# Optimization experiments

Measured on AMD Instinct MI355X. Metric: run time of the kernel, lower is better.

The kernel has to match this reference:

```python
import jax, jax.numpy as jnp
import numpy as np

B, S, D, H = 4, 2048, 1024, 16
HS = D // H  # head size = 64


def setup_inputs() -> dict:
    key = jax.random.key(0)
    k1, k2, k3 = jax.random.split(key, 3)
    return {
        "input_data": jax.random.normal(k1, (B, S, D), dtype=jnp.float32),
        "w_qkv": jax.random.normal(k2, (D, 3 * D), dtype=jnp.float32) * (1.0 / np.sqrt(D)),
        "b_qkv": jnp.zeros((3 * D,), dtype=jnp.float32),
        "w_proj": jax.random.normal(k3, (D, D), dtype=jnp.float32) * (1.0 / np.sqrt(D)),
        "b_proj": jnp.zeros((D,), dtype=jnp.float32),
    }


def reference(input_data, w_qkv, b_qkv, w_proj, b_proj):
    b, s, d = input_data.shape
    qkv = input_data @ w_qkv + b_qkv  # [b, s, 3d]
    q, k, v = jnp.split(qkv, 3, axis=-1)
    # [b, h, s, hs]
    q = q.reshape(b, s, H, HS).transpose(0, 2, 1, 3)
    k = k.reshape(b, s, H, HS).transpose(0, 2, 1, 3)
    v = v.reshape(b, s, H, HS).transpose(0, 2, 1, 3)
    # NB: original module scales by 1/sqrt(num_heads), not 1/sqrt(head_size)
    scores = jnp.einsum('bhqd,bhkd->bhqk', q, k) / jnp.sqrt(jnp.float32(H))
    causal = jnp.tril(jnp.ones((s, s), dtype=bool))
    scores = jnp.where(causal[None, None], scores, -jnp.inf)
    weights = jax.nn.softmax(scores, axis=-1)  # dropout p=0.0 -> identity
    out = jnp.einsum('bhqk,bhkd->bhqd', weights, v)
    out = out.transpose(0, 2, 1, 3).reshape(b, s, d)
    return out @ w_proj + b_proj
```

## Files before the change

### kernel.cpp

```cpp
#include <hip/hip_runtime.h>


typedef unsigned short u16;
typedef short bf16x8 __attribute__((ext_vector_type(8)));
typedef unsigned short u16x8 __attribute__((ext_vector_type(8)));
typedef float f32x4 __attribute__((ext_vector_type(4)));
typedef float f32x16 __attribute__((ext_vector_type(16)));

#define S_LEN 2048
#define DMODEL 1024
#define NHEAD 16
#define MROWS 8192

#define SCALE_LOG2E 0.36067376022224085f
#define DEFER_THR 8.0f

__device__ __forceinline__ u16 f2bf(float f) {
  union { float f; unsigned u; } c; c.f = f;
  unsigned u = c.u;
  u += 0x7fffu + ((u >> 16) & 1u);
  return (u16)(u >> 16);
}

__device__ __forceinline__ float exp2_fast(float x) {
  float r; asm("v_exp_f32 %0, %1" : "=v"(r) : "v"(x)); return r;
}

__device__ __forceinline__ unsigned cvtpk_bf16(float a, float b) {
  unsigned r;
  asm("v_cvt_pk_bf16_f32 %0, %1, %2" : "=v"(r) : "v"(a), "v"(b));
  return r;
}

__device__ __forceinline__ void plswap(unsigned& a, unsigned& b) {
  asm("v_permlane32_swap_b32 %0, %1" : "+v"(a), "+v"(b));
}

__device__ __forceinline__ f32x4 mfma16(bf16x8 a, bf16x8 b, f32x4 c) {
  return __builtin_amdgcn_mfma_f32_16x16x32_bf16(a, b, c, 0, 0, 0);
}

__device__ __forceinline__ f32x16 mfma32(bf16x8 a, bf16x8 b, f32x16 c) {
  return __builtin_amdgcn_mfma_f32_32x32x16_bf16(a, b, c, 0, 0, 0);
}

__device__ __forceinline__ void gload_lds16(const void* g, void* l) {
  __builtin_amdgcn_global_load_lds((__attribute__((address_space(1))) void*)g,
                                   (__attribute__((address_space(3))) void*)l,
                                   16, 0, 0);
}

__global__ void k_f32_to_bf16(const float* __restrict__ in, u16* __restrict__ out, int n) {
  int i = (blockIdx.x * 256 + threadIdx.x) * 4;
  if (i < n) {
    float4 v = *reinterpret_cast<const float4*>(in + i);
    ushort4 o;
    o.x = f2bf(v.x); o.y = f2bf(v.y); o.z = f2bf(v.z); o.w = f2bf(v.w);
    *reinterpret_cast<ushort4*>(out + i) = o;
  }
}

__global__ void k_transpose_to_bf16(const float* __restrict__ in, u16* __restrict__ out,
                                    int K, int N) {
  __shared__ float t[32][33];
  int n0 = blockIdx.x * 32, k0 = blockIdx.y * 32;
  int tx = threadIdx.x & 31, ty = threadIdx.x >> 5;
#pragma unroll
  for (int i = 0; i < 32; i += 8)
    t[ty + i][tx] = in[(size_t)(k0 + ty + i) * N + n0 + tx];
  __syncthreads();
#pragma unroll
  for (int i = 0; i < 32; i += 8)
    out[(size_t)(n0 + ty + i) * K + k0 + tx] = f2bf(t[tx][ty + i]);
}

template <int MODE>
__global__ __launch_bounds__(256) void k_gemm_bt(const u16* __restrict__ A,
                                                 const u16* __restrict__ Bt,
                                                 const float* __restrict__ bias,
                                                 u16* __restrict__ outb,
                                                 float* __restrict__ outf,
                                                 u16* __restrict__ vtout,
                                                 int N, int K) {
  __shared__ u16 As[128 * 64];
  __shared__ u16 Bs[128 * 64];
  const int tid = threadIdx.x;
  const int lane = tid & 63, wave = tid >> 6;
  const int wm = wave >> 1, wn = wave & 1;
  const int lr = lane & 15, lk = lane >> 4;
  const int m0 = blockIdx.x * 128, n0 = blockIdx.y * 128;

  f32x4 zero4 = {0.f, 0.f, 0.f, 0.f};
  f32x4 acc[4][4];
#pragma unroll
  for (int m = 0; m < 4; ++m)
#pragma unroll
    for (int n = 0; n < 4; ++n) acc[m][n] = zero4;

  const int nkt = K >> 6;
  for (int kt = 0; kt < nkt; ++kt) {
    const u16* Ag = A + (size_t)m0 * K + kt * 64;
    const u16* Bg = Bt + (size_t)n0 * K + kt * 64;
#pragma unroll
    for (int j = 0; j < 4; ++j) {
      int chunk = j * 4 + wave;
      int row = chunk * 8 + (lane >> 3);
      int cole = (lane & 7) * 8;
      gload_lds16(Ag + (size_t)row * K + cole, &As[chunk * 512]);
      gload_lds16(Bg + (size_t)row * K + cole, &Bs[chunk * 512]);
    }
    __syncthreads();
#pragma unroll
    for (int ks = 0; ks < 2; ++ks) {
      bf16x8 af[4], bfr[4];
#pragma unroll
      for (int m = 0; m < 4; ++m)
        af[m] = *reinterpret_cast<const bf16x8*>(&As[(wm * 64 + m * 16 + lr) * 64 + ks * 32 + lk * 8]);
#pragma unroll
      for (int n = 0; n < 4; ++n)
        bfr[n] = *reinterpret_cast<const bf16x8*>(&Bs[(wn * 64 + n * 16 + lr) * 64 + ks * 32 + lk * 8]);
#pragma unroll
      for (int m = 0; m < 4; ++m)
#pragma unroll
        for (int n = 0; n < 4; ++n) acc[m][n] = mfma16(af[m], bfr[n], acc[m][n]);
    }
    __syncthreads();
  }

#pragma unroll
  for (int n = 0; n < 4; ++n) {
    int col = n0 + wn * 64 + n * 16 + lr;
    float bv = bias[col];
#pragma unroll
    for (int m = 0; m < 4; ++m) {
      int rowb = m0 + wm * 64 + m * 16 + lk * 4;
      if (MODE == 1) {
#pragma unroll
        for (int r = 0; r < 4; ++r)
          outf[(size_t)(rowb + r) * N + col] = acc[m][n][r] + bv;
      } else {
        if (col < 2048) {
#pragma unroll
          for (int r = 0; r < 4; ++r)
            outb[(size_t)(rowb + r) * 2048 + col] = f2bf(acc[m][n][r] + bv);
        } else {
          int hh = (col >> 6) & 15, dd = col & 63;
          int bb = rowb >> 11, ss = rowb & 2047;
          ushort4 o;
          o.x = f2bf(acc[m][n][0] + bv);
          o.y = f2bf(acc[m][n][1] + bv);
          o.z = f2bf(acc[m][n][2] + bv);
          o.w = f2bf(acc[m][n][3] + bv);
          *reinterpret_cast<ushort4*>(
              vtout + ((size_t)(bb * 16 + hh) * 64 + dd) * 2048 + ss) = o;
        }
      }
    }
  }
}

__global__ __launch_bounds__(256, 2) void k_attn5(const u16* __restrict__ qk,
                                                  const u16* __restrict__ vt,
                                                  u16* __restrict__ ao) {
  __shared__ u16 Ks[2][4096];
  __shared__ u16 Vs[2][4096];

  const int tid = threadIdx.x;
  const int lane = tid & 63, wave = tid >> 6;
  const int l31 = lane & 31, hi = lane >> 5;
  const int gid = blockIdx.x;
  const int bh = gid & 63;
  const int tq = gid >> 6;
  const int qb = (tq < 4) ? tq : 11 - tq;
  const int b = bh >> 4, h = bh & 15;

  const int qlo0 = qb * 128 + wave * 32;
  const int qhi0 = 1920 - qb * 128 + wave * 32;
  const int ktd_lo = qlo0 >> 6;
  const int ktd_hi = qhi0 >> 6;
  const int KTMAX = 31 - 2 * qb;
  const int qrel0 = qlo0 + l31 - ktd_lo * 64;
  const int qrel1 = qhi0 + l31 - ktd_hi * 64;

  bf16x8 qf[2][4];
  {
    const u16* q0p = qk + ((size_t)b * S_LEN + qlo0 + l31) * 2048 + h * 64 + hi * 8;
    const u16* q1p = qk + ((size_t)b * S_LEN + qhi0 + l31) * 2048 + h * 64 + hi * 8;
#pragma unroll
    for (int ks = 0; ks < 4; ++ks) {
      qf[0][ks] = *reinterpret_cast<const bf16x8*>(q0p + ks * 16);
      qf[1][ks] = *reinterpret_cast<const bf16x8*>(q1p + ks * 16);
    }
  }

  const int swzcol = 16 * ((lane & 7) ^ (lane >> 3));
  const char* kg = (const char*)qk + ((size_t)b * S_LEN) * 4096 + 2048 + h * 128 +
                   (size_t)(lane >> 3) * 4096 + swzcol;
  const char* vg = (const char*)vt + ((size_t)bh * 64 + (lane >> 3)) * 4096 + swzcol;

#define STAGE(BUF, KT)                                                              \
  {                                                                                 \
    const char* kg_ = kg + (size_t)(KT) * 64 * 4096;                                \
    const char* vg_ = vg + (size_t)(KT) * 128;                                      \
    gload_lds16(kg_ + (size_t)(wave * 8) * 4096, &Ks[BUF][wave * 512]);             \
    gload_lds16(kg_ + (size_t)((wave + 4) * 8) * 4096, &Ks[BUF][(wave + 4) * 512]); \
    gload_lds16(vg_ + (size_t)(wave * 8) * 4096, &Vs[BUF][wave * 512]);             \
    gload_lds16(vg_ + (size_t)((wave + 4) * 8) * 4096, &Vs[BUF][(wave + 4) * 512]); \
  }

  f32x16 oT[2][2];
#pragma unroll
  for (int m = 0; m < 2; ++m)
#pragma unroll
    for (int kb = 0; kb < 2; ++kb)
#pragma unroll
      for (int g = 0; g < 16; ++g) oT[m][kb][g] = 0.f;
  float m_i[2] = {-INFINITY, -INFINITY};
  float l_i[2] = {0.f, 0.f};

  const int rsw = (l31 & 7) << 4;

#define SM32(SC, M, MASKED, QREL, FR)                                           \
  {                                                                             \
    float s_[2][16];                                                            \
    float mx_ = -INFINITY;                                                      \
    _Pragma("unroll") for (int kb = 0; kb < 2; ++kb)                            \
      _Pragma("unroll") for (int g = 0; g < 16; ++g) {                          \
        float v_ = SC[kb][g] * SCALE_LOG2E;                                     \
        if (MASKED) {                                                           \
          int key_ = kb * 32 + (g & 3) + ((g >> 2) << 3) + hi * 4;              \
          if (key_ > (QREL)) v_ = -INFINITY;                                    \
        }                                                                       \
        s_[kb][g] = v_;                                                         \
        mx_ = fmaxf(mx_, v_);                                                   \
      }                                                                         \
    mx_ = fmaxf(mx_, __shfl_xor(mx_, 32, 64));                                  \
    if (__any(mx_ > m_i[M] + DEFER_THR)) {                                      \
      float mn_ = fmaxf(m_i[M], mx_);                                           \
      float c_ = exp2_fast(m_i[M] - mn_);                                       \
      m_i[M] = mn_;                                                             \
      l_i[M] *= c_;                                                             \
      _Pragma("unroll") for (int kb = 0; kb < 2; ++kb)                          \
        _Pragma("unroll") for (int g = 0; g < 16; ++g) oT[M][kb][g] *= c_;      \
    }                                                                           \
    float rs_ = 0.f;                                                            \
    unsigned pk_[8][2];                                                         \
    _Pragma("unroll") for (int kb = 0; kb < 2; ++kb)                            \
      _Pragma("unroll") for (int s = 0; s < 4; ++s) {                           \
        float p0_ = exp2_fast(s_[kb][s * 4 + 0] - m_i[M]);                      \
        float p1_ = exp2_fast(s_[kb][s * 4 + 1] - m_i[M]);                      \
        float p2_ = exp2_fast(s_[kb][s * 4 + 2] - m_i[M]);                      \
        float p3_ = exp2_fast(s_[kb][s * 4 + 3] - m_i[M]);                      \
        rs_ += (p0_ + p1_) + (p2_ + p3_);                                       \
        pk_[kb * 4 + s][0] = cvtpk_bf16(p0_, p1_);                              \
        pk_[kb * 4 + s][1] = cvtpk_bf16(p2_, p3_);                              \
      }                                                                         \
    rs_ += __shfl_xor(rs_, 32, 64);                                             \
    l_i[M] += rs_;                                                              \
    _Pragma("unroll") for (int t = 0; t < 4; ++t) {                             \
      unsigned a0_ = pk_[2 * t][0], b0_ = pk_[2 * t + 1][0];                    \
      unsigned a1_ = pk_[2 * t][1], b1_ = pk_[2 * t + 1][1];                    \
      plswap(a0_, b0_);                                                         \
      plswap(a1_, b1_);                                                         \
      FR[t][0] = a0_; FR[t][1] = a1_; FR[t][2] = b0_; FR[t][3] = b1_;           \
    }                                                                           \
  }

  STAGE(0, 0);
  __syncthreads();
  int buf = 0;

  for (int kt = 0; kt <= KTMAX; ++kt) {
    if (kt < KTMAX) STAGE(buf ^ 1, kt + 1);

    const char* Kb = (const char*)&Ks[buf][0];
    const char* Vb = (const char*)&Vs[buf][0];
    const bool lo_act = (kt <= ktd_lo);
    const bool hi_act = (kt <= ktd_hi);
    const bool mask0 = (kt == ktd_lo), mask1 = (kt == ktd_hi);

    bf16x8 kf[2][4];
#pragma unroll
    for (int kb = 0; kb < 2; ++kb)
#pragma unroll
      for (int ks = 0; ks < 4; ++ks)
        kf[kb][ks] = *reinterpret_cast<const bf16x8*>(
            Kb + (kb * 32 + l31) * 128 + ((ks * 32 + hi * 16) ^ rsw));

    f32x16 sc0[2], sc1[2];
#pragma unroll
    for (int kb = 0; kb < 2; ++kb) {
      if (hi_act) {
        sc1[kb] = mfma32(kf[kb][0], qf[1][0], f32x16{});
#pragma unroll
        for (int ks = 1; ks < 4; ++ks) sc1[kb] = mfma32(kf[kb][ks], qf[1][ks], sc1[kb]);
      }
      if (lo_act) {
        sc0[kb] = mfma32(kf[kb][0], qf[0][0], f32x16{});
#pragma unroll
        for (int ks = 1; ks < 4; ++ks) sc0[kb] = mfma32(kf[kb][ks], qf[0][ks], sc0[kb]);
      }
    }

    bf16x8 vf[2][4];
#pragma unroll
    for (int kbd = 0; kbd < 2; ++kbd)
#pragma unroll
      for (int t = 0; t < 4; ++t)
        vf[kbd][t] = *reinterpret_cast<const bf16x8*>(
            Vb + (kbd * 32 + l31) * 128 + ((t * 32 + hi * 16) ^ rsw));

    if (lo_act) {
      unsigned fr0[4][4];
      SM32(sc0, 0, mask0, qrel0, fr0);
#pragma unroll
      for (int t = 0; t < 4; ++t) {
        bf16x8 pb = *reinterpret_cast<const bf16x8*>(&fr0[t][0]);
        oT[0][0] = mfma32(vf[0][t], pb, oT[0][0]);
        oT[0][1] = mfma32(vf[1][t], pb, oT[0][1]);
      }
    }
    if (hi_act) {
      unsigned fr1[4][4];
      SM32(sc1, 1, mask1, qrel1, fr1);
#pragma unroll
      for (int t = 0; t < 4; ++t) {
        bf16x8 pb = *reinterpret_cast<const bf16x8*>(&fr1[t][0]);
        oT[1][0] = mfma32(vf[0][t], pb, oT[1][0]);
        oT[1][1] = mfma32(vf[1][t], pb, oT[1][1]);
      }
    }

    __syncthreads();
    buf ^= 1;
  }
#undef SM32
#undef STAGE

#pragma unroll
  for (int m = 0; m < 2; ++m) {
    const int qbase = (m == 0) ? qlo0 : qhi0;
    float inv = 1.f / l_i[m];
    u16* orow = ao + ((size_t)b * S_LEN + qbase + l31) * DMODEL + h * 64 + hi * 4;
#pragma unroll
    for (int kbd = 0; kbd < 2; ++kbd)
#pragma unroll
      for (int s = 0; s < 4; ++s) {
        unsigned w0 = cvtpk_bf16(oT[m][kbd][s * 4 + 0] * inv, oT[m][kbd][s * 4 + 1] * inv);
        unsigned w1 = cvtpk_bf16(oT[m][kbd][s * 4 + 2] * inv, oT[m][kbd][s * 4 + 3] * inv);
        *reinterpret_cast<unsigned*>(orow + kbd * 32 + s * 8) = w0;
        *reinterpret_cast<unsigned*>(orow + kbd * 32 + s * 8 + 2) = w1;
      }
  }
}

extern "C" void kernel_launch(void* const* d_in, const int* in_sizes, int n_in,
                              void* d_out, int out_size, void* d_ws, size_t ws_size,
                              hipStream_t stream) {
  const float* x = (const float*)d_in[0];
  const float* wqkv = (const float*)d_in[1];
  const float* bqkv = (const float*)d_in[2];
  const float* wproj = (const float*)d_in[3];
  const float* bproj = (const float*)d_in[4];
  float* out = (float*)d_out;

  char* ws = (char*)d_ws;
  u16* Xb     = (u16*)(ws);
  u16* Wqkvt  = (u16*)(ws + (size_t)16777216);
  u16* Wprojt = (u16*)(ws + (size_t)23068672);
  u16* QKb    = (u16*)(ws + (size_t)25165824);
  u16* Vt     = (u16*)(ws + (size_t)58720256);
  u16* AOb    = (u16*)(ws + (size_t)75497472);

  k_f32_to_bf16<<<MROWS * DMODEL / 4 / 256, 256, 0, stream>>>(x, Xb, MROWS * DMODEL);
  k_transpose_to_bf16<<<dim3(3072 / 32, 1024 / 32), 256, 0, stream>>>(wqkv, Wqkvt, 1024, 3072);
  k_transpose_to_bf16<<<dim3(1024 / 32, 1024 / 32), 256, 0, stream>>>(wproj, Wprojt, 1024, 1024);

  k_gemm_bt<2><<<dim3(MROWS / 128, 3072 / 128), 256, 0, stream>>>(
      Xb, Wqkvt, bqkv, QKb, nullptr, Vt, 3072, 1024);

  k_attn5<<<dim3(512), 256, 0, stream>>>(QKb, Vt, AOb);

  k_gemm_bt<1><<<dim3(MROWS / 128, DMODEL / 128), 256, 0, stream>>>(
      AOb, Wprojt, bproj, nullptr, out, nullptr, DMODEL, 1024);
}
```

Baseline: 199.5 us.

## Rewrite GEMM as 8-wave double-buffered pipeline with swizzled LDS and 256x128 tiles

Replaces the 4-wave 128x128 GEMM with a 512-thread kernel that computes 256x128 tiles. It double-buffers LDS in K-halves so the next tile's global-to-LDS loads overlap the current MFMAs. It uses an XOR-swizzled LDS layout to avoid bank conflicts, and waits with fine-grained vmcnt plus setprio around the MFMA blocks. This targets global-load latency and LDS conflicts in both projection GEMMs. The cost is more LDS and registers per block and fewer blocks per launch, which may reduce occupancy on the smaller output projection.

Result: faster. 184.8 us (-7.4%).

```diff
diff --git a/kernel.cpp b/kernel.cpp
--- a/kernel.cpp
+++ b/kernel.cpp
@@ -75,20 +75,35 @@
 }
 
 template <int MODE>
-__global__ __launch_bounds__(256) void k_gemm_bt(const u16* __restrict__ A,
-                                                 const u16* __restrict__ Bt,
-                                                 const float* __restrict__ bias,
-                                                 u16* __restrict__ outb,
-                                                 float* __restrict__ outf,
-                                                 u16* __restrict__ vtout,
-                                                 int N, int K) {
-  __shared__ u16 As[128 * 64];
-  __shared__ u16 Bs[128 * 64];
+__global__ __launch_bounds__(512, 1) void k_gemm8(const u16* __restrict__ A,
+                                                  const u16* __restrict__ Bt,
+                                                  const float* __restrict__ bias,
+                                                  u16* __restrict__ outb,
+                                                  float* __restrict__ outf,
+                                                  u16* __restrict__ vtout,
+                                                  int N, int K) {
+  __shared__ u16 As[2][2][256 * 32];
+  __shared__ u16 Bs[2][2][128 * 32];
+
   const int tid = threadIdx.x;
   const int lane = tid & 63, wave = tid >> 6;
-  const int wm = wave >> 1, wn = wave & 1;
+  const int wr = wave >> 1, wc = wave & 1;
   const int lr = lane & 15, lk = lane >> 4;
-  const int m0 = blockIdx.x * 128, n0 = blockIdx.y * 128;
+  const int m0 = blockIdx.x * 256, n0 = blockIdx.y * 128;
+  const size_t Kb = (size_t)K * 2;
+
+  const int csw = ((tid & 3) ^ ((tid >> 3) & 3)) * 16;
+  const char* Asrc0 = (const char*)A + (size_t)(m0 + (tid >> 2)) * Kb + csw;
+  const char* Asrc1 = Asrc0 + 128 * Kb;
+  const char* Bsrc0 = (const char*)Bt + (size_t)(n0 + (tid >> 2)) * Kb + csw;
+
+#define STAGE_KH(BUFX, KH, T)                                                  \
+  {                                                                            \
+    const size_t ko_ = (size_t)(T) * 128 + (KH) * 64;                          \
+    gload_lds16(Asrc0 + ko_, &As[BUFX][KH][(size_t)tid * 8]);                  \
+    gload_lds16(Asrc1 + ko_, &As[BUFX][KH][((size_t)tid + 512) * 8]);          \
+    gload_lds16(Bsrc0 + ko_, &Bs[BUFX][KH][(size_t)tid * 8]);                  \
+  }
 
   f32x4 zero4 = {0.f, 0.f, 0.f, 0.f};
   f32x4 acc[4][4];
@@ -97,43 +112,54 @@
 #pragma unroll
     for (int n = 0; n < 4; ++n) acc[m][n] = zero4;
 
+  const int slotsw = (lr >> 1) & 3;
+
+#define PHASE(BUFX, KH, T, DOSTAGE, VMZERO)                                    \
+  {                                                                            \
+    if (VMZERO) asm volatile("s_waitcnt vmcnt(0)" ::: "memory");               \
+    else        asm volatile("s_waitcnt vmcnt(3)" ::: "memory");               \
+    __builtin_amdgcn_s_barrier();                                              \
+    __builtin_amdgcn_sched_barrier(0);                                         \
+    bf16x8 af[4], bfr[4];                                                      \
+    _Pragma("unroll") for (int m = 0; m < 4; ++m)                              \
+        af[m] = *reinterpret_cast<const bf16x8*>(                              \
+            &As[BUFX][KH][(wr * 64 + m * 16 + lr) * 32 + ((lk ^ slotsw) * 8)]);\
+    _Pragma("unroll") for (int n = 0; n < 4; ++n)                              \
+        bfr[n] = *reinterpret_cast<const bf16x8*>(                             \
+            &Bs[BUFX][KH][(wc * 64 + n * 16 + lr) * 32 + ((lk ^ slotsw) * 8)]);\
+    if (DOSTAGE) STAGE_KH((BUFX) ^ 1, KH, (T) + 1);                            \
+    __builtin_amdgcn_sched_barrier(0);                                         \
+    __builtin_amdgcn_s_setprio(1);                                             \
+    _Pragma("unroll") for (int m = 0; m < 4; ++m)                              \
+        _Pragma("unroll") for (int n = 0; n < 4; ++n)                          \
+            acc[m][n] = mfma16(af[m], bfr[n], acc[m][n]);                      \
+    __builtin_amdgcn_s_setprio(0);                                             \
+  }
+
   const int nkt = K >> 6;
-  for (int kt = 0; kt < nkt; ++kt) {
-    const u16* Ag = A + (size_t)m0 * K + kt * 64;
-    const u16* Bg = Bt + (size_t)n0 * K + kt * 64;
-#pragma unroll
-    for (int j = 0; j < 4; ++j) {
-      int chunk = j * 4 + wave;
-      int row = chunk * 8 + (lane >> 3);
-      int cole = (lane & 7) * 8;
-      gload_lds16(Ag + (size_t)row * K + cole, &As[chunk * 512]);
-      gload_lds16(Bg + (size_t)row * K + cole, &Bs[chunk * 512]);
-    }
-    __syncthreads();
-#pragma unroll
-    for (int ks = 0; ks < 2; ++ks) {
-      bf16x8 af[4], bfr[4];
-#pragma unroll
-      for (int m = 0; m < 4; ++m)
-        af[m] = *reinterpret_cast<const bf16x8*>(&As[(wm * 64 + m * 16 + lr) * 64 + ks * 32 + lk * 8]);
-#pragma unroll
-      for (int n = 0; n < 4; ++n)
-        bfr[n] = *reinterpret_cast<const bf16x8*>(&Bs[(wn * 64 + n * 16 + lr) * 64 + ks * 32 + lk * 8]);
-#pragma unroll
-      for (int m = 0; m < 4; ++m)
-#pragma unroll
-        for (int n = 0; n < 4; ++n) acc[m][n] = mfma16(af[m], bfr[n], acc[m][n]);
-    }
-    __syncthreads();
-  }
+  STAGE_KH(0, 0, 0);
+  STAGE_KH(0, 1, 0);
+
+  for (int t = 0; t < nkt - 1; ++t) {
+    const int buf = t & 1;
+    PHASE(buf, 0, t, 1, 0);
+    PHASE(buf, 1, t, 1, 0);
+  }
+  {
+    const int buf = (nkt - 1) & 1;
+    PHASE(buf, 0, nkt - 1, 0, 0);
+    PHASE(buf, 1, nkt - 1, 0, 1);
+  }
+#undef PHASE
+#undef STAGE_KH
 
 #pragma unroll
   for (int n = 0; n < 4; ++n) {
-    int col = n0 + wn * 64 + n * 16 + lr;
+    int col = n0 + wc * 64 + n * 16 + lr;
     float bv = bias[col];
 #pragma unroll
     for (int m = 0; m < 4; ++m) {
-      int rowb = m0 + wm * 64 + m * 16 + lk * 4;
+      int rowb = m0 + wr * 64 + m * 16 + lk * 4;
       if (MODE == 1) {
 #pragma unroll
         for (int r = 0; r < 4; ++r)
@@ -376,11 +402,11 @@
   k_transpose_to_bf16<<<dim3(3072 / 32, 1024 / 32), 256, 0, stream>>>(wqkv, Wqkvt, 1024, 3072);
   k_transpose_to_bf16<<<dim3(1024 / 32, 1024 / 32), 256, 0, stream>>>(wproj, Wprojt, 1024, 1024);
 
-  k_gemm_bt<2><<<dim3(MROWS / 128, 3072 / 128), 256, 0, stream>>>(
+  k_gemm8<2><<<dim3(MROWS / 256, 3072 / 128), 512, 0, stream>>>(
       Xb, Wqkvt, bqkv, QKb, nullptr, Vt, 3072, 1024);
 
   k_attn5<<<dim3(512), 256, 0, stream>>>(QKb, Vt, AOb);
 
-  k_gemm_bt<1><<<dim3(MROWS / 128, DMODEL / 128), 256, 0, stream>>>(
+  k_gemm8<1><<<dim3(MROWS / 256, DMODEL / 128), 512, 0, stream>>>(
       AOb, Wprojt, bproj, nullptr, out, nullptr, DMODEL, 1024);
 }
```
